# Performance work log

Hardware: AMD Instinct MI355X
Metric: run time of the kernel (lower is better)

## Reference

```python
import jax, jax.numpy as jnp
import numpy as np

HIDDEN = 32
WINDOW = 128
ALPHA = 2.5
T_LEN = 524288


def setup_inputs() -> dict:
    key = jax.random.key(0)
    ks = jax.random.split(key, 9)
    H = HIDDEN
    s = 1.0 / np.sqrt(H)
    u = lambda k, shape: jax.random.uniform(k, shape, jnp.float32, -s, s)
    return {
        "x": jax.random.normal(ks[0], (1, T_LEN, 1), jnp.float32),
        "Wih": u(ks[1], (3 * H, 2)),
        "Whh": u(ks[2], (3 * H, H)),
        "bih": u(ks[3], (3 * H,)),
        "bhh": u(ks[4], (3 * H,)),
        "Wv": u(ks[5], (H, 1)),
        "bv": u(ks[6], (1,)),
        "Ws": u(ks[7], (H, 1)),
        "bs": u(ks[8], (1,)),
    }


def _spike_mask(x1):
    """Vectorized replacement of the per-timestep Python loop.
    mask[t] True iff |x[t] - (2x[t-1]-x[t-2])| > alpha*(sqrt(mean(x[max(0,t-W):t]^2))+1e-8).
    Uses a prefix sum of x^2 for the sliding-window mean. mask[0]=mask[1]=True."""
    T = x1.shape[0]
    cs = jnp.concatenate([jnp.zeros((1,), x1.dtype), jnp.cumsum(x1 * x1)])  # [T+1]
    t = jnp.arange(T)
    ws = jnp.maximum(0, t - WINDOW)
    cnt = jnp.maximum(t - ws, 1).astype(x1.dtype)
    rms = jnp.sqrt(jnp.maximum(cs[t] - cs[ws], 0.0) / cnt) + 1e-8
    pred = 2.0 * jnp.roll(x1, 1) - jnp.roll(x1, 2)  # garbage at t<2, overwritten below
    err = jnp.abs(x1 - pred)
    mask = err > (ALPHA * rms)
    return mask.at[:2].set(True)


def _gru_cell(inp, h, Wih, Whh, bih, bhh):
    H = h.shape[0]
    gi = Wih @ inp + bih  # [3H]
    gh = Whh @ h + bhh    # [3H]
    r = jax.nn.sigmoid(gi[:H] + gh[:H])
    z = jax.nn.sigmoid(gi[H:2 * H] + gh[H:2 * H])
    n = jnp.tanh(gi[2 * H:] + r * gh[2 * H:])
    return (1.0 - z) * n + z * h


def reference(x, Wih, Whh, bih, bhh, Wv, bv, Ws, bs):
    x1 = x[0, :, 0]                       # [T]
    T = x1.shape[0]
    mask = _spike_mask(x1)                # [T] bool (non-differentiable, as in torch detach)
    tf = jnp.arange(T, dtype=x1.dtype)

    # GRU state is only updated at event steps (equivalent to running the GRU over the
    # compacted event sequence); between events the held state is used for linear
    # extrapolation val + slope * (t - t_event)/window.
    def step(carry, inp):
        h, last_t = carry
        xt, m, t = inp
        delta = (t - last_t) / float(WINDOW)
        h_new = _gru_cell(jnp.stack([xt, delta]), h, Wih, Whh, bih, bhh)
        h = jnp.where(m, h_new, h)
        last_t = jnp.where(m, t, last_t)
        dt = (t - last_t) / float(WINDOW)  # 0 at event steps
        out = (h @ Wv + bv) + (h @ Ws + bs) * dt  # [1]
        return (h, last_t), out[0]

    init = (jnp.zeros((HIDDEN,), x1.dtype), jnp.zeros((), x1.dtype))
    _, outs = jax.lax.scan(step, init, (x1, mask, tf))
    output = outs.reshape(1, T, 1)
    N = jnp.sum(mask.astype(jnp.int32))
    return output, N, mask
```

## Files before the change

kernel.cpp:

```cpp
#include <hip/hip_runtime.h>
#include <stdint.h>

#define T_LEN 524288
#define SEG 8
#define WARM 8
#define EPC (SEG + WARM + 1)
#define CHAINS 16
#define GSP (CHAINS * SEG)
#define CBLK 1536
#define NCH 512

typedef short short8 __attribute__((ext_vector_type(8)));
typedef float f4 __attribute__((ext_vector_type(4)));
#define KEEPA(v) asm volatile("" : "+v"(v))

static const size_t OFF_MASK = 0;
static const size_t OFF_CNT  = T_LEN;

__device__ __forceinline__ short bfr(float f) {
    uint32_t u = __float_as_uint(f);
    u = (u + 0x7fffu + ((u >> 16) & 1u)) >> 16;
    return (short)u;
}

#define IDX(j) ((j) + ((j) >> 5))

__global__ __launch_bounds__(256) void k_mask(const float* __restrict__ x,
                                              uint8_t* __restrict__ mask,
                                              float* __restrict__ out, int out_size,
                                              int* __restrict__ cnt)
{
    __shared__ float tile[1190];
    __shared__ float cs2[1190];
    __shared__ float wsum[4];
    __shared__ int tot;
    const int bs = blockIdx.x * 1024;
    const int tid = threadIdx.x;
    const int lane = tid & 63, w = tid >> 6;
    if (tid == 0) tot = 0;
    for (int j = tid; j < 1154; j += 256) {
        int g = bs - 130 + j;
        tile[IDX(j)] = (g >= 0) ? x[g] : 0.f;
    }
    __syncthreads();

    const int j0 = tid * 5;
    float p[5];
    float run = 0.f;
    #pragma unroll
    for (int k = 0; k < 5; ++k) {
        float v = (j0 + k < 1154) ? tile[IDX(j0 + k)] : 0.f;
        run = fmaf(v, v, run);
        p[k] = run;
    }
    float incl = run;
    for (int d = 1; d < 64; d <<= 1) {
        float u = __shfl_up(incl, d, 64);
        if (lane >= d) incl += u;
    }
    if (lane == 63) wsum[w] = incl;
    __syncthreads();
    float base = incl - run;
    for (int i = 0; i < w; ++i) base += wsum[i];
    #pragma unroll
    for (int k = 0; k < 5; ++k)
        if (j0 + k < 1154) cs2[IDX(j0 + k)] = base + p[k];
    __syncthreads();

    const int loc = tid * 4;
    float tv[6];
    #pragma unroll
    for (int q = 0; q < 6; ++q) tv[q] = tile[IDX(loc + 128 + q)];
    uchar4 mv; float4 mf; int msum = 0;
    uint8_t* mp = &mv.x; float* fp = &mf.x;
    #pragma unroll
    for (int it = 0; it < 4; ++it) {
        int t = bs + loc + it;
        int c = t < 128 ? (t < 1 ? 1 : t) : 128;
        float s = cs2[IDX(loc + 129 + it)] - cs2[IDX(loc + 1 + it)];
        float rms = sqrtf(fmaxf(s, 0.f) / (float)c) + 1e-8f;
        float xt = tv[it + 2];
        float pr = 2.f * tv[it + 1] - tv[it];
        bool m = (t < 2) || (fabsf(xt - pr) > 2.5f * rms);
        mp[it] = m ? 1 : 0; fp[it] = m ? 1.f : 0.f; msum += m ? 1 : 0;
    }
    *(uchar4*)(mask + bs + loc) = mv;
    int oi = T_LEN + 1 + bs + loc;
    if (oi + 3 < out_size) *(float4*)(out + oi) = mf;
    for (int d = 32; d; d >>= 1) msum += __shfl_down(msum, d, 64);
    if ((tid & 63) == 0) atomicAdd(&tot, msum);
    __syncthreads();
    if (tid == 0) cnt[blockIdx.x] = tot;
}

__global__ __attribute__((amdgpu_waves_per_eu(2)))
__launch_bounds__(64)
void k_chain(const float* __restrict__ Whh,
             const float* __restrict__ Wih,
             const float* __restrict__ bih,
             const float* __restrict__ bhh,
             const uint8_t* __restrict__ mask,
             const int* __restrict__ cnt,
             const float* __restrict__ x,
             const float* __restrict__ Wv,
             const float* __restrict__ bv,
             const float* __restrict__ Wsc,
             const float* __restrict__ bs,
             float* __restrict__ out, int out_size)
{
    __shared__ float2   st[CHAINS * EPC];
    __shared__ unsigned hx[CHAINS * 20];
    __shared__ float    ab[2 * GSP];
    __shared__ int      P[NCH + 1];
    __shared__ int      tn_sh;

    const int lane = threadIdx.x;
    const int m = lane & 15;
    const int quad = lane >> 4;

    int vv[8]; int locs = 0;
    #pragma unroll
    for (int k = 0; k < 8; ++k) { vv[k] = cnt[lane * 8 + k]; locs += vv[k]; }
    int incp = locs;
    for (int d = 1; d < 64; d <<= 1) {
        int u = __shfl_up(incp, d, 64);
        if (lane >= d) incp += u;
    }
    int runp = incp - locs;
    #pragma unroll
    for (int k = 0; k < 8; ++k) { P[lane * 8 + k] = runp; runp += vv[k]; }
    if (lane == 63) P[NCH] = incp;
    __builtin_amdgcn_wave_barrier();
    const int N = P[NCH];
    if (blockIdx.x == 0 && lane == 0 && T_LEN < out_size) out[T_LEN] = (float)N;

    short8 A1[6], A2[6], A3;
    #pragma unroll
    for (int t = 0; t < 6; ++t) {
        union { short s[8]; short8 v; } u1, u2;
        int rowg = 16 * t + m;
        #pragma unroll
        for (int j = 0; j < 8; ++j) {
            int k = 8 * quad + j;
            u1.s[j] = bfr(Whh[rowg * 32 + k]);
            float a2v = 0.f;
            if (k == 0) a2v = Wih[rowg * 2];
            else if (k == 1) a2v = Wih[rowg * 2 + 1];
            else if (k == 2) a2v = (rowg < 64) ? (bih[rowg] + bhh[rowg]) : bih[rowg];
            u2.s[j] = bfr(a2v);
        }
        A1[t] = u1.v; A2[t] = u2.v;
    }
    {
        union { short s[8]; short8 v; } u3;
        #pragma unroll
        for (int j = 0; j < 8; ++j) {
            int k = 8 * quad + j;
            float v = (m == 0) ? Wv[k] : (m == 1) ? Wsc[k] : 0.f;
            u3.s[j] = bfr(v);
        }
        A3 = u3.v;
    }
    #pragma unroll
    for (int t = 0; t < 6; ++t) { KEEPA(A1[t]); KEEPA(A2[t]); }
    KEEPA(A3);

    float bn0[4], bn1[4];
    #pragma unroll
    for (int e = 0; e < 4; ++e) {
        int r0 = quad * 4 + e;
        bn0[e] = bhh[64 + r0];  bn1[e] = bhh[80 + r0];
    }
    const float bv0 = bv[0], bs0 = bs[0];

    for (int g0 = blockIdx.x; g0 * GSP < N; g0 += CBLK) {
        const int base0 = g0 * GSP;
        const int s_lo = base0 - (WARM + 1);
        const int s_hi = base0 + GSP;
        const int s_lo_c = max(s_lo, 0);
        const int s_hi_c = min(s_hi, N - 1);

        if (lane == 0) tn_sh = T_LEN;
        if (s_lo < 0) {
            float x0 = x[0];
            for (int e = lane; e < CHAINS * EPC; e += 64) {
                int n = e / EPC, j = e - n * EPC;
                int s = base0 + n * SEG - (WARM + 1) + j;
                if (s < 0) st[e] = make_float2(0.f, x0);
            }
        }

        int c0 = -1, c1 = -1;
        #pragma unroll
        for (int k = 0; k < 8; ++k) {
            int c = lane * 8 + k;
            if (P[c] <= s_lo_c && s_lo_c < P[c + 1]) c0 = c;
            if (P[c] <= s_hi_c && s_hi_c < P[c + 1]) c1 = c;
        }
        for (int d = 32; d; d >>= 1) {
            c0 = max(c0, __shfl_down(c0, d, 64));
            c1 = max(c1, __shfl_down(c1, d, 64));
        }
        c0 = __shfl(c0, 0, 64);
        c1 = __shfl(c1, 0, 64);

        for (int c = c0; c <= c1; ++c) {
            const uint8_t* mp = mask + c * 1024 + lane * 16;
            uint4 mw = *(const uint4*)mp;
            int cl = __popc(mw.x) + __popc(mw.y) + __popc(mw.z) + __popc(mw.w);
            int ic = cl;
            for (int d = 1; d < 64; d <<= 1) {
                int u = __shfl_up(ic, d, 64);
                if (lane >= d) ic += u;
            }
            int s = P[c] + ic - cl;
            unsigned wds[4] = {mw.x, mw.y, mw.z, mw.w};
            #pragma unroll
            for (int wq = 0; wq < 4; ++wq) {
                unsigned W = wds[wq];
                #pragma unroll
                for (int by = 0; by < 4; ++by) {
                    if ((W >> (8 * by)) & 1u) {
                        if (s >= s_lo_c && s <= s_hi_c) {
                            int t = c * 1024 + lane * 16 + wq * 4 + by;
                            int rel = s - base0;
                            if (rel == GSP) {
                                tn_sh = t;
                            } else {
                                float xv = x[t];
                                int n_lo = rel >> 3;
                                int n_hi = (rel + 9) >> 3;
                                n_lo = max(n_lo, 0); n_hi = min(n_hi, CHAINS - 1);
                                for (int n = n_lo; n <= n_hi; ++n) {
                                    int j = rel + (WARM + 1) - SEG * n;
                                    st[n * EPC + j] = make_float2((float)t, xv);
                                }
                            }
                        }
                        ++s;
                    }
                }
            }
        }
        __builtin_amdgcn_wave_barrier();
        const int tN = tn_sh;

        float h0[4], h1[4];
        #pragma unroll
        for (int e = 0; e < 4; ++e) { h0[e] = 0.f; h1[e] = 0.f; }
        short8 B1 = (short8)0;
        float tprev = st[m * EPC].x;

        for (int j = 0; j < SEG + WARM; ++j) {
            float2 cur = st[m * EPC + j + 1];
            float xt = cur.y;
            float d = (cur.x - tprev) * 0.0078125f;
            tprev = cur.x;

            unsigned p0 = (__float_as_uint(d) & 0xFFFF0000u) | (__float_as_uint(xt) >> 16);
            unsigned p1 = 0x00003F80u;
            p0 = (quad == 0) ? p0 : 0u;
            p1 = (quad == 0) ? p1 : 0u;
            union { unsigned u[4]; short8 v; } b2u;
            b2u.u[0] = p0; b2u.u[1] = p1; b2u.u[2] = 0u; b2u.u[3] = 0u;
            short8 B2 = b2u.v;

            f4 z4 = {0.f, 0.f, 0.f, 0.f};
            f4 Drz[4], Dh0, Dh1, Di0, Di1;
            f4 tmp0 = __builtin_amdgcn_mfma_f32_16x16x32_bf16(A2[0], B2, z4, 0, 0, 0);
            f4 tmp1 = __builtin_amdgcn_mfma_f32_16x16x32_bf16(A2[1], B2, z4, 0, 0, 0);
            f4 tmp2 = __builtin_amdgcn_mfma_f32_16x16x32_bf16(A2[2], B2, z4, 0, 0, 0);
            f4 tmp3 = __builtin_amdgcn_mfma_f32_16x16x32_bf16(A2[3], B2, z4, 0, 0, 0);
            Di0 = __builtin_amdgcn_mfma_f32_16x16x32_bf16(A2[4], B2, z4, 0, 0, 0);
            Di1 = __builtin_amdgcn_mfma_f32_16x16x32_bf16(A2[5], B2, z4, 0, 0, 0);
            Drz[0] = __builtin_amdgcn_mfma_f32_16x16x32_bf16(A1[0], B1, tmp0, 0, 0, 0);
            Drz[1] = __builtin_amdgcn_mfma_f32_16x16x32_bf16(A1[1], B1, tmp1, 0, 0, 0);
            Drz[2] = __builtin_amdgcn_mfma_f32_16x16x32_bf16(A1[2], B1, tmp2, 0, 0, 0);
            Drz[3] = __builtin_amdgcn_mfma_f32_16x16x32_bf16(A1[3], B1, tmp3, 0, 0, 0);
            Dh0 = __builtin_amdgcn_mfma_f32_16x16x32_bf16(A1[4], B1, z4, 0, 0, 0);
            Dh1 = __builtin_amdgcn_mfma_f32_16x16x32_bf16(A1[5], B1, z4, 0, 0, 0);

            #pragma unroll
            for (int e = 0; e < 4; ++e) {
                float r0 = __builtin_amdgcn_rcpf(1.f + __builtin_amdgcn_exp2f(-1.44269504089f * Drz[0][e]));
                float r1 = __builtin_amdgcn_rcpf(1.f + __builtin_amdgcn_exp2f(-1.44269504089f * Drz[1][e]));
                float zz0 = __builtin_amdgcn_rcpf(1.f + __builtin_amdgcn_exp2f(-1.44269504089f * Drz[2][e]));
                float zz1 = __builtin_amdgcn_rcpf(1.f + __builtin_amdgcn_exp2f(-1.44269504089f * Drz[3][e]));
                float np0 = fmaf(r0, Dh0[e] + bn0[e], Di0[e]);
                float np1 = fmaf(r1, Dh1[e] + bn1[e], Di1[e]);
                float en0 = __builtin_amdgcn_exp2f(2.88539008178f * np0);
                float en1 = __builtin_amdgcn_exp2f(2.88539008178f * np1);
                float n0 = fmaf(-2.f, __builtin_amdgcn_rcpf(1.f + en0), 1.f);
                float n1 = fmaf(-2.f, __builtin_amdgcn_rcpf(1.f + en1), 1.f);
                h0[e] = fmaf(zz0, h0[e] - n0, n0);
                h1[e] = fmaf(zz1, h1[e] - n1, n1);
            }

            unsigned q0 = (__float_as_uint(h0[1]) & 0xFFFF0000u) | (__float_as_uint(h0[0]) >> 16);
            unsigned q1 = (__float_as_uint(h0[3]) & 0xFFFF0000u) | (__float_as_uint(h0[2]) >> 16);
            unsigned q2 = (__float_as_uint(h1[1]) & 0xFFFF0000u) | (__float_as_uint(h1[0]) >> 16);
            unsigned q3 = (__float_as_uint(h1[3]) & 0xFFFF0000u) | (__float_as_uint(h1[2]) >> 16);
            *(uint2*)&hx[m * 20 + 2 * quad]     = make_uint2(q0, q1);
            *(uint2*)&hx[m * 20 + 8 + 2 * quad] = make_uint2(q2, q3);
            __builtin_amdgcn_wave_barrier();
            union { uint4 u; short8 v; } bu;
            bu.u = *(const uint4*)&hx[m * 20 + 4 * quad];
            B1 = bu.v;

            if (j >= WARM) {
                f4 Dab = __builtin_amdgcn_mfma_f32_16x16x32_bf16(A3, B1, z4, 0, 0, 0);
                if (quad == 0) {
                    int sg = base0 + m * SEG + (j - WARM);
                    if (sg < N)
                        *(float2*)&ab[2 * (m * SEG + j - WARM)] =
                            make_float2(Dab[0] + bv0, Dab[1] + bs0);
                }
            }
        }
        __builtin_amdgcn_wave_barrier();

        #pragma unroll
        for (int h = 0; h < 2; ++h) {
            int sl = lane + 64 * h;
            int sg = base0 + sl;
            if (sg < N) {
                int n = sl >> 3, jj = sl & 7;
                float ts = st[n * EPC + (WARM + 1) + jj].x;
                int tnext;
                if (sg + 1 >= N) tnext = T_LEN;
                else if (sl + 1 < GSP) {
                    int n2 = (sl + 1) >> 3, j2 = (sl + 1) & 7;
                    tnext = (int)st[n2 * EPC + (WARM + 1) + j2].x;
                } else tnext = tN;
                float2 abv = *(const float2*)&ab[2 * sl];
                int tsi = (int)ts;
                for (int t = tsi; t < tnext; ++t)
                    out[t] = fmaf(abv.y, (float)(t - tsi) * 0.0078125f, abv.x);
            }
        }
        __builtin_amdgcn_wave_barrier();
    }
}

extern "C" void kernel_launch(void* const* d_in, const int* in_sizes, int n_in,
                              void* d_out, int out_size, void* d_ws, size_t ws_size,
                              hipStream_t stream)
{
    const float* x   = (const float*)d_in[0];
    const float* Wih = (const float*)d_in[1];
    const float* Whh = (const float*)d_in[2];
    const float* bih = (const float*)d_in[3];
    const float* bhh = (const float*)d_in[4];
    const float* Wv  = (const float*)d_in[5];
    const float* bv  = (const float*)d_in[6];
    const float* Wsc = (const float*)d_in[7];
    const float* bs  = (const float*)d_in[8];
    float* out = (float*)d_out;

    char* ws = (char*)d_ws;
    uint8_t* mask = (uint8_t*)(ws + OFF_MASK);
    int* cnt  = (int*)(ws + OFF_CNT);

    k_mask<<<512, 256, 0, stream>>>(x, mask, out, out_size, cnt);
    k_chain<<<CBLK, 64, 0, stream>>>(Whh, Wih, bih, bhh, mask, cnt, x,
                                     Wv, bv, Wsc, bs, out, out_size);
}
```

Baseline: 108.8 us.

## Emit compacted per-block spike index lists instead of byte mask

The mask kernel now performs a block-level prefix scan and writes the time indices of events into per-chunk compacted lists. The chain kernel no longer scans 1024-byte mask chunks with popcounts and shuffles to locate events; each lane directly looks up the needed event indices via the chunk prefix and a short linear search. This removes the serial mask-decoding pass per group, at the cost of scattered int writes in the mask kernel and an uncoalesced gather of x[t].

```diff
diff --git a/kernel.cpp b/kernel.cpp
--- a/kernel.cpp
+++ b/kernel.cpp
@@ -14,8 +14,8 @@
 typedef float f4 __attribute__((ext_vector_type(4)));
 #define KEEPA(v) asm volatile("" : "+v"(v))
 
-static const size_t OFF_MASK = 0;
-static const size_t OFF_CNT  = T_LEN;
+static const size_t OFF_CNT = 0;
+static const size_t OFF_SPK = 8192;
 
 __device__ __forceinline__ short bfr(float f) {
     uint32_t u = __float_as_uint(f);
@@ -26,18 +26,17 @@
 #define IDX(j) ((j) + ((j) >> 5))
 
 __global__ __launch_bounds__(256) void k_mask(const float* __restrict__ x,
-                                              uint8_t* __restrict__ mask,
                                               float* __restrict__ out, int out_size,
-                                              int* __restrict__ cnt)
+                                              int* __restrict__ cnt,
+                                              int* __restrict__ spk)
 {
     __shared__ float tile[1190];
     __shared__ float cs2[1190];
     __shared__ float wsum[4];
-    __shared__ int tot;
+    __shared__ int wtot[4];
     const int bs = blockIdx.x * 1024;
     const int tid = threadIdx.x;
     const int lane = tid & 63, w = tid >> 6;
-    if (tid == 0) tot = 0;
     for (int j = tid; j < 1154; j += 256) {
         int g = bs - 130 + j;
         tile[IDX(j)] = (g >= 0) ? x[g] : 0.f;
@@ -71,8 +70,8 @@
     float tv[6];
     #pragma unroll
     for (int q = 0; q < 6; ++q) tv[q] = tile[IDX(loc + 128 + q)];
-    uchar4 mv; float4 mf; int msum = 0;
-    uint8_t* mp = &mv.x; float* fp = &mf.x;
+    float4 mf; int mbit[4]; int msum = 0;
+    float* fp = &mf.x;
     #pragma unroll
     for (int it = 0; it < 4; ++it) {
         int t = bs + loc + it;
@@ -82,15 +81,28 @@
         float xt = tv[it + 2];
         float pr = 2.f * tv[it + 1] - tv[it];
         bool m = (t < 2) || (fabsf(xt - pr) > 2.5f * rms);
-        mp[it] = m ? 1 : 0; fp[it] = m ? 1.f : 0.f; msum += m ? 1 : 0;
-    }
-    *(uchar4*)(mask + bs + loc) = mv;
+        mbit[it] = m ? 1 : 0; fp[it] = m ? 1.f : 0.f; msum += m ? 1 : 0;
+    }
     int oi = T_LEN + 1 + bs + loc;
     if (oi + 3 < out_size) *(float4*)(out + oi) = mf;
-    for (int d = 32; d; d >>= 1) msum += __shfl_down(msum, d, 64);
-    if ((tid & 63) == 0) atomicAdd(&tot, msum);
+
+    int e1 = mbit[0], e2 = mbit[0] + mbit[1], e3 = e2 + mbit[2];
+    int incs = msum;
+    for (int d = 1; d < 64; d <<= 1) {
+        int u = __shfl_up(incs, d, 64);
+        if (lane >= d) incs += u;
+    }
+    if (lane == 63) wtot[w] = incs;
     __syncthreads();
-    if (tid == 0) cnt[blockIdx.x] = tot;
+    int woff = 0;
+    for (int i = 0; i < w; ++i) woff += wtot[i];
+    int texcl = woff + incs - msum;
+    int ee[4] = {0, e1, e2, e3};
+    int* sp = spk + blockIdx.x * 1024 + texcl;
+    #pragma unroll
+    for (int k = 0; k < 4; ++k)
+        if (mbit[k]) sp[ee[k]] = bs + loc + k;
+    if (tid == 0) cnt[blockIdx.x] = wtot[0] + wtot[1] + wtot[2] + wtot[3];
 }
 
 __global__ __attribute__((amdgpu_waves_per_eu(2)))
@@ -99,7 +111,7 @@
              const float* __restrict__ Wih,
              const float* __restrict__ bih,
              const float* __restrict__ bhh,
-             const uint8_t* __restrict__ mask,
+             const int* __restrict__ spk,
              const int* __restrict__ cnt,
              const float* __restrict__ x,
              const float* __restrict__ Wv,
@@ -175,71 +187,33 @@
 
     for (int g0 = blockIdx.x; g0 * GSP < N; g0 += CBLK) {
         const int base0 = g0 * GSP;
-        const int s_lo = base0 - (WARM + 1);
-        const int s_hi = base0 + GSP;
-        const int s_lo_c = max(s_lo, 0);
-        const int s_hi_c = min(s_hi, N - 1);
-
-        if (lane == 0) tn_sh = T_LEN;
-        if (s_lo < 0) {
-            float x0 = x[0];
-            for (int e = lane; e < CHAINS * EPC; e += 64) {
-                int n = e / EPC, j = e - n * EPC;
-                int s = base0 + n * SEG - (WARM + 1) + j;
-                if (s < 0) st[e] = make_float2(0.f, x0);
-            }
-        }
-
-        int c0 = -1, c1 = -1;
+        const int s_lo_c = max(base0 - (WARM + 1), 0);
+
+        int c0 = -1;
         #pragma unroll
         for (int k = 0; k < 8; ++k) {
             int c = lane * 8 + k;
             if (P[c] <= s_lo_c && s_lo_c < P[c + 1]) c0 = c;
-            if (P[c] <= s_hi_c && s_hi_c < P[c + 1]) c1 = c;
-        }
-        for (int d = 32; d; d >>= 1) {
-            c0 = max(c0, __shfl_down(c0, d, 64));
-            c1 = max(c1, __shfl_down(c1, d, 64));
-        }
-        c0 = __shfl(c0, 0, 64);
-        c1 = __shfl(c1, 0, 64);
-
-        for (int c = c0; c <= c1; ++c) {
-            const uint8_t* mp = mask + c * 1024 + lane * 16;
-            uint4 mw = *(const uint4*)mp;
-            int cl = __popc(mw.x) + __popc(mw.y) + __popc(mw.z) + __popc(mw.w);
-            int ic = cl;
-            for (int d = 1; d < 64; d <<= 1) {
-                int u = __shfl_up(ic, d, 64);
-                if (lane >= d) ic += u;
-            }
-            int s = P[c] + ic - cl;
-            unsigned wds[4] = {mw.x, mw.y, mw.z, mw.w};
-            #pragma unroll
-            for (int wq = 0; wq < 4; ++wq) {
-                unsigned W = wds[wq];
-                #pragma unroll
-                for (int by = 0; by < 4; ++by) {
-                    if ((W >> (8 * by)) & 1u) {
-                        if (s >= s_lo_c && s <= s_hi_c) {
-                            int t = c * 1024 + lane * 16 + wq * 4 + by;
-                            int rel = s - base0;
-                            if (rel == GSP) {
-                                tn_sh = t;
-                            } else {
-                                float xv = x[t];
-                                int n_lo = rel >> 3;
-                                int n_hi = (rel + 9) >> 3;
-                                n_lo = max(n_lo, 0); n_hi = min(n_hi, CHAINS - 1);
-                                for (int n = n_lo; n <= n_hi; ++n) {
-                                    int j = rel + (WARM + 1) - SEG * n;
-                                    st[n * EPC + j] = make_float2((float)t, xv);
-                                }
-                            }
-                        }
-                        ++s;
-                    }
-                }
+        }
+        for (int d = 32; d; d >>= 1) c0 = max(c0, __shfl_down(c0, d, 64));
+        const int c0w = __shfl(c0, 0, 64);
+
+        for (int e = lane; e < CHAINS * EPC; e += 64) {
+            int n = e / EPC, j = e - n * EPC;
+            int s = base0 + n * SEG - (WARM + 1) + j;
+            s = min(max(s, 0), N - 1);
+            int c = c0w;
+            while (P[c + 1] <= s) ++c;
+            int t = spk[c * 1024 + (s - P[c])];
+            st[e] = make_float2((float)t, x[t]);
+        }
+        if (lane == 0) {
+            int nid = base0 + GSP;
+            if (nid >= N) tn_sh = T_LEN;
+            else {
+                int c = c0w;
+                while (P[c + 1] <= nid) ++c;
+                tn_sh = spk[c * 1024 + (nid - P[c])];
             }
         }
         __builtin_amdgcn_wave_barrier();
@@ -358,10 +332,10 @@
     float* out = (float*)d_out;
 
     char* ws = (char*)d_ws;
-    uint8_t* mask = (uint8_t*)(ws + OFF_MASK);
-    int* cnt  = (int*)(ws + OFF_CNT);
-
-    k_mask<<<512, 256, 0, stream>>>(x, mask, out, out_size, cnt);
-    k_chain<<<CBLK, 64, 0, stream>>>(Whh, Wih, bih, bhh, mask, cnt, x,
+    int* cnt = (int*)(ws + OFF_CNT);
+    int* spk = (int*)(ws + OFF_SPK);
+
+    k_mask<<<512, 256, 0, stream>>>(x, out, out_size, cnt, spk);
+    k_chain<<<CBLK, 64, 0, stream>>>(Whh, Wih, bih, bhh, spk, cnt, x,
                                      Wv, bv, Wsc, bs, out, out_size);
 }
```

After: 102.7 us. 5.6% less time.
